# Kernel optimization log

Measured on AMD Instinct MI355X. Metric: run time of the kernel, lower is better.

Reference implementation:

```python
import jax, jax.numpy as jnp
import numpy as np

V, E, H = 50000, 256, 256   # vocab, emb_dim, hid_dim
R, S, W = 64, 32, 64        # reviews, sentences/review, words/sentence
UF = 20                     # user feature dim


def _bigru_last(x, wih, whh, bih, bhh):
    """Bidirectional GRU over x [B,T,D]; returns sum of final hidden states of
    the two directions, shape [B,H]. Params stacked over direction axis 0."""
    Hh = whh.shape[-1]

    def onedir(xd, wi, wh, bi, bh):
        gx = jnp.einsum('btd,gd->btg', xd, wi) + bi  # [B,T,3H] input gates precomputed

        def step(h, gxt):
            gh = h @ wh.T + bh
            r = jax.nn.sigmoid(gxt[:, :Hh] + gh[:, :Hh])
            z = jax.nn.sigmoid(gxt[:, Hh:2 * Hh] + gh[:, Hh:2 * Hh])
            n = jnp.tanh(gxt[:, 2 * Hh:] + r * gh[:, 2 * Hh:])
            return (1.0 - z) * n + z * h, None

        h0 = jnp.zeros((xd.shape[0], Hh), xd.dtype)
        hT, _ = jax.lax.scan(step, h0, jnp.swapaxes(gx, 0, 1))
        return hT

    return (onedir(x, wih[0], whh[0], bih[0], bhh[0])
            + onedir(x[:, ::-1], wih[1], whh[1], bih[1], bhh[1]))


def setup_inputs() -> dict:
    key = jax.random.key(0)
    ks = iter(jax.random.split(key, 40))

    def wmat(shape, scale=0.05):
        return jax.random.normal(next(ks), shape, jnp.float32) * scale

    inp = {}
    inp['inputs'] = jax.random.randint(next(ks), (R, S, W), 0, V)
    inp['sent_lengths'] = jax.random.randint(next(ks), (R, S), 1, W)
    inp['sent_counts'] = jax.random.randint(next(ks), (R,), 1, S)
    inp['user_feats'] = jax.random.normal(next(ks), (R, UF), jnp.float32)
    inp['embed'] = wmat((V, E))
    for name, din in (('wg', E), ('sg', H), ('rg', H + UF)):
        inp[name + '_wih'] = wmat((2, 3 * H, din))
        inp[name + '_whh'] = wmat((2, 3 * H, H))
        inp[name + '_bih'] = jnp.zeros((2, 3 * H), jnp.float32)
        inp[name + '_bhh'] = jnp.zeros((2, 3 * H), jnp.float32)
    inp['rfc_w1'] = wmat((H // 2, H + UF)); inp['rfc_b1'] = jnp.zeros((H // 2,), jnp.float32)
    inp['rfc_w2'] = wmat((1, H // 2));      inp['rfc_b2'] = jnp.zeros((1,), jnp.float32)
    inp['pfc_w1'] = wmat((H // 2, H));      inp['pfc_b1'] = jnp.zeros((H // 2,), jnp.float32)
    inp['pfc_w2'] = wmat((9, H // 2));      inp['pfc_b2'] = jnp.zeros((9,), jnp.float32)
    inp['uf_w'] = jnp.ones((UF,), jnp.float32)  # user_feats_weights
    return inp


def reference(inputs, sent_lengths, sent_counts, user_feats, embed,
              wg_wih, wg_whh, wg_bih, wg_bhh,
              sg_wih, sg_whh, sg_bih, sg_bhh,
              rg_wih, rg_whh, rg_bih, rg_bhh,
              rfc_w1, rfc_b1, rfc_w2, rfc_b2,
              pfc_w1, pfc_b1, pfc_w2, pfc_b2, uf_w):
    Rr, Sr, Wr = inputs.shape
    emb = embed[inputs]  # [R,S,W,E]  (dropout = identity in eval mode)
    # word-level bi-GRU, all R*S sentences batched together
    sent = _bigru_last(emb.reshape(Rr * Sr, Wr, emb.shape[-1]),
                       wg_wih, wg_whh, wg_bih, wg_bhh).reshape(Rr, Sr, -1)
    # sentence-level bi-GRU, batch over reviews
    rev = _bigru_last(sent, sg_wih, sg_whh, sg_bih, sg_bhh)  # [R,H]
    # F.normalize(user_feats) * user_feats_weights
    nrm = jnp.maximum(jnp.linalg.norm(user_feats, axis=-1, keepdims=True), 1e-12)
    p_batch = jnp.concatenate([rev, (user_feats / nrm) * uf_w], axis=-1)  # [R,H+20]
    r_stars = (jax.nn.selu(p_batch @ rfc_w1.T + rfc_b1) @ rfc_w2.T + rfc_b2)[:, 0]  # [R]
    # review-level bi-GRU over the sequence of reviews (batch 1)
    doc = _bigru_last(p_batch[None], rg_wih, rg_whh, rg_bih, rg_bhh)[0]  # [H]
    p_stars = jax.nn.selu(doc @ pfc_w1.T + pfc_b1) @ pfc_w2.T + pfc_b2  # [9]
    return p_stars, r_stars
```

## Files before the change

kernel.cpp:

```cpp
#include <hip/hip_runtime.h>
#include <math.h>

#define R_ 64
#define S_ 32
#define W_ 64
#define H_ 256
#define UF_ 20
#define TC 4

typedef short bf16x8 __attribute__((ext_vector_type(8)));
typedef float f32x4  __attribute__((ext_vector_type(4)));

#define MFMA(a,b,c) __builtin_amdgcn_mfma_f32_16x16x32_bf16((a),(b),(c),0,0,0)

#define BFRAG(ff) ((ff) < 40 ? Breg[(ff) < 40 ? (ff) : 0] \
                 : *(const bf16x8*)&Bl[w][(ff) >= 40 ? (ff)-40 : 0][l*8])

__device__ __forceinline__ float sigf(float x){ return 1.0f/(1.0f+__expf(-x)); }
__device__ __forceinline__ float tanhf_(float x){ float e=__expf(2.0f*x); return 1.0f-2.0f/(e+1.0f); }
__device__ __forceinline__ float seluf_(float x){
  const float sc=1.0507009873554805f, al=1.6732632423543772f;
  return x>0.0f ? sc*x : sc*al*(expf(x)-1.0f);
}
__device__ __forceinline__ short tobf(float f){
  unsigned u=__float_as_uint(f); u += 0x7fffu + ((u>>16)&1u); return (short)(u>>16);
}
__device__ __forceinline__ float bf2f(short s){
  return __uint_as_float(((unsigned)(unsigned short)s) << 16);
}
__device__ __forceinline__ unsigned pk2(float a, float b){
  return (unsigned)(unsigned short)tobf(a) | ((unsigned)(unsigned short)tobf(b) << 16);
}

__global__ void prep_word_w(const float* __restrict__ wih, const float* __restrict__ whh,
                            short* __restrict__ Bw)
{
  int idx = blockIdx.x*256 + threadIdx.x;
  int lane = idx & 63;
  int rest = idx >> 6;
  int f  = rest % 6;  rest /= 6;
  int kt = rest % 16; rest /= 16;
  int w  = rest % 8;
  int d  = rest / 8;
  int gate = f >> 1;
  int j = 32*w + (f&1)*16 + (lane&15);
  int row = gate*256 + j;
  const float* W = (kt < 8 ? wih : whh) + (size_t)d*768*256;
  int k = (kt&7)*32 + (lane>>4)*8;
  short* dst = Bw + ((((size_t)(d*8 + w)*16 + kt)*6 + f)*64 + lane)*8;
#pragma unroll
  for (int jj=0;jj<8;jj++) dst[jj] = tobf(W[(size_t)row*256 + k + jj]);
}

__global__ void prep_rnn_w(const float* __restrict__ whh, short* __restrict__ Bs)
{
  int idx = blockIdx.x*256 + threadIdx.x;
  int lane = idx & 63;
  int rest = idx >> 6;
  int f  = rest % 6; rest /= 6;
  int kt = rest % 8; rest /= 8;
  int w  = rest % 8;
  int d  = rest / 8;
  int j = 32*w + (f&1)*16 + (lane&15);
  int row = (f>>1)*256 + j;
  const float* W = whh + (size_t)d*768*256;
  int k = kt*32 + (lane>>4)*8;
  short* dst = Bs + ((((size_t)(d*8 + w)*8 + kt)*6 + f)*64 + lane)*8;
#pragma unroll
  for (int jj=0;jj<8;jj++) dst[jj] = tobf(W[(size_t)row*256 + k + jj]);
}

__global__ void prep_gemm_w(const float* __restrict__ Wsrc, short* __restrict__ Bg)
{
  int idx = blockIdx.x*256 + threadIdx.x;
  int lane = idx & 63;
  int rest = idx >> 6;
  int kt = rest % 8;
  int nt = rest / 8;
  int n = nt*16 + (lane&15);
  int k = kt*32 + (lane>>4)*8;
  short* dst = Bg + (((size_t)nt*8 + kt)*64 + lane)*8;
#pragma unroll
  for (int jj=0;jj<8;jj++) dst[jj] = tobf(Wsrc[(size_t)n*256 + k + jj]);
}

__global__ __launch_bounds__(256) void gemm_gxu(
    const short* __restrict__ Ab, const float* __restrict__ Af,
    const int* __restrict__ toks, const short* __restrict__ Bg,
    const float* __restrict__ bih, const float* __restrict__ bhh,
    short* __restrict__ C, long Czoff,
    int mode, int t0, int Mclamp, int Cstride)
{
  const int z  = blockIdx.z;
  const int m0 = blockIdx.x * 64;
  const int yt = blockIdx.y * 8;
  const int ntb = (mode == 2 ? z*48 : 0) + yt;
  const int tid = threadIdx.x;
  const int w = tid >> 6, l = tid & 63;
  const int c = l & 15, q = l >> 4;
  __shared__ short As[64][264];
  {
    const int row = tid >> 2, c0 = (tid & 3) * 64;
    if (mode == 0) {
      const uint4* s = (const uint4*)(Ab + (size_t)(m0+row)*256 + c0);
#pragma unroll
      for (int i = 0; i < 8; i++) *(uint4*)&As[row][c0 + i*8] = s[i];
    } else {
      int r;
      if (mode == 1) {
        r = m0 + row; if (r >= Mclamp) r = Mclamp - 1;
      } else {
        const int rr = m0 + row;
        const int s_ = rr / TC, i_ = rr % TC;
        const int wd = z ? (63 - (t0 + i_)) : (t0 + i_);
        r = toks[s_*64 + wd];
      }
      const float* s = Af + (size_t)r*256 + c0;
#pragma unroll
      for (int i = 0; i < 8; i++) {
        float4 v0 = *(const float4*)(s + i*8);
        float4 v1 = *(const float4*)(s + i*8 + 4);
        uint4 u;
        u.x = pk2(v0.x, v0.y); u.y = pk2(v0.z, v0.w);
        u.z = pk2(v1.x, v1.y); u.w = pk2(v1.z, v1.w);
        *(uint4*)&As[row][c0 + i*8] = u;
      }
    }
  }
  float bias[2];
#pragma unroll
  for (int nt = 0; nt < 2; nt++) {
    const int coln = (yt + 2*w + nt)*16 + c;
    const int bidx = (mode == 2 ? z*768 : 0) + coln;
    bias[nt] = bih[bidx] + ((bidx % 768) < 512 ? bhh[bidx] : 0.0f);
  }
  __syncthreads();
  f32x4 acc[4][2];
#pragma unroll
  for (int a = 0; a < 4; a++) { acc[a][0] = (f32x4)0.f; acc[a][1] = (f32x4)0.f; }
#pragma unroll
  for (int kt = 0; kt < 8; kt++) {
    const int ko = kt*32 + q*8;
    bf16x8 a0 = *(const bf16x8*)&As[ 0+c][ko];
    bf16x8 a1 = *(const bf16x8*)&As[16+c][ko];
    bf16x8 a2 = *(const bf16x8*)&As[32+c][ko];
    bf16x8 a3 = *(const bf16x8*)&As[48+c][ko];
    bf16x8 b0 = *(const bf16x8*)&Bg[(((size_t)(ntb + 2*w    )*8 + kt)*64 + l)*8];
    bf16x8 b1 = *(const bf16x8*)&Bg[(((size_t)(ntb + 2*w + 1)*8 + kt)*64 + l)*8];
    acc[0][0]=MFMA(a0,b0,acc[0][0]); acc[1][0]=MFMA(a1,b0,acc[1][0]);
    acc[2][0]=MFMA(a2,b0,acc[2][0]); acc[3][0]=MFMA(a3,b0,acc[3][0]);
    acc[0][1]=MFMA(a0,b1,acc[0][1]); acc[1][1]=MFMA(a1,b1,acc[1][1]);
    acc[2][1]=MFMA(a2,b1,acc[2][1]); acc[3][1]=MFMA(a3,b1,acc[3][1]);
  }
  short* Cz = C + (size_t)z * Czoff;
#pragma unroll
  for (int mt = 0; mt < 4; mt++)
#pragma unroll
  for (int nt = 0; nt < 2; nt++)
#pragma unroll
  for (int rg = 0; rg < 4; rg++)
    Cz[(size_t)(m0 + mt*16 + q*4 + rg)*Cstride + (yt + 2*w + nt)*16 + c] =
        tobf(acc[mt][nt][rg] + bias[nt]);
}

__global__ __launch_bounds__(512, 2) void gru_rec(
    const int* __restrict__ toks,
    const short* __restrict__ gxF, const short* __restrict__ gxB,
    const short* __restrict__ Bh, int wstride, int koff,
    const float* __restrict__ bhh,
    float* __restrict__ hstate, int NS,
    int t0, int nsteps, int mode, int nwords)
{
  const int d = blockIdx.x & 1;
  const int g = blockIdx.x >> 1;
  const int tid = threadIdx.x;
  const int w = tid >> 6, l = tid & 63;
  const int c = l & 15, q = l >> 4;
  const int j0 = 32*w + c;

  __shared__ short hbf[2][16][256];
  __shared__ short Bl[8][8][512];
  __shared__ int   tokL[1024];

  if (mode == 0)
    for (int i = tid; i < 1024; i += 512) tokL[i] = toks[(size_t)g*1024 + i];

  bf16x8 Breg[40];
  {
    const short* Bb = Bh + (size_t)(d*8 + w)*wstride + (size_t)koff*3072 + l*8;
#pragma unroll
    for (int ff = 0; ff < 48; ff++) {
      bf16x8 v = *(const bf16x8*)(Bb + ff*512);
      if (ff < 40) Breg[ff] = v;
      else *(bf16x8*)&Bl[w][ff-40][l*8] = v;
    }
  }

  float bNH[2];
#pragma unroll
  for (int jt = 0; jt < 2; jt++)
    bNH[jt] = bhh[d*768 + 512 + j0 + jt*16];

  float hst[2][4];
  const int cur0 = t0 & 1;
  if (t0 == 0) {
#pragma unroll
    for (int a = 0; a < 2; a++)
#pragma unroll
    for (int r = 0; r < 4; r++) hst[a][r] = 0.0f;
  } else {
#pragma unroll
    for (int jt = 0; jt < 2; jt++)
#pragma unroll
    for (int rg = 0; rg < 4; rg++)
      hst[jt][rg] = hstate[((size_t)d*NS + g*16 + q*4 + rg)*256 + j0 + jt*16];
  }
#pragma unroll
  for (int jt = 0; jt < 2; jt++)
#pragma unroll
  for (int rg = 0; rg < 4; rg++) {
    const int m = q*4 + rg;
    hbf[cur0][m][(j0 + jt*16) ^ ((m&7)<<3)] = tobf(hst[jt][rg]);
  }

  __syncthreads();

  const int tend = t0 + nsteps;
  for (int t = t0; t < tend; t++) {
    const int cur = t & 1, nxt = 1 - cur;

    const short* rb[4];
#pragma unroll
    for (int rg = 0; rg < 4; rg++) {
      const int m = q*4 + rg;
      if (mode == 0) {
        const int tx = d ? (nwords - 1 - t) : t;
        rb[rg] = gxF + (size_t)tokL[m*64 + tx]*1536 + d*768 + j0;
      } else if (mode == 1) {
        const int ri = (g*16 + m)*TC + (t - t0);
        rb[rg] = (d ? gxB : gxF) + (size_t)ri*768 + j0;
      } else {
        const int se = d ? (nwords - 1 - t) : t;
        rb[rg] = gxF + ((size_t)(g*16 + m)*nwords + se)*1536 + d*768 + j0;
      }
    }
    short Gv[4][2][3];
#pragma unroll
    for (int rg = 0; rg < 4; rg++)
#pragma unroll
    for (int jt = 0; jt < 2; jt++)
#pragma unroll
    for (int ga = 0; ga < 3; ga++)
      Gv[rg][jt][ga] = rb[rg][ga*256 + jt*16];

    f32x4 accR[2], accZ[2], accNH[2];
#pragma unroll
    for (int a = 0; a < 2; a++) { accR[a]=(f32x4)0.f; accZ[a]=(f32x4)0.f; accNH[a]=(f32x4)0.f; }
#pragma unroll
    for (int kt = 0; kt < 8; kt++) {
      bf16x8 a0 = *(const bf16x8*)&hbf[cur][c][(kt*32 + q*8) ^ ((c&7)<<3)];
      bf16x8 b0 = BFRAG(kt*6+0), b1 = BFRAG(kt*6+1), b2 = BFRAG(kt*6+2),
             b3 = BFRAG(kt*6+3), b4 = BFRAG(kt*6+4), b5 = BFRAG(kt*6+5);
      accR[0]=MFMA(a0,b0,accR[0]);  accR[1]=MFMA(a0,b1,accR[1]);
      accZ[0]=MFMA(a0,b2,accZ[0]);  accZ[1]=MFMA(a0,b3,accZ[1]);
      accNH[0]=MFMA(a0,b4,accNH[0]); accNH[1]=MFMA(a0,b5,accNH[1]);
    }

#pragma unroll
    for (int jt = 0; jt < 2; jt++)
#pragma unroll
    for (int rg = 0; rg < 4; rg++) {
      const int m = q*4 + rg;
      const float r = sigf(bf2f(Gv[rg][jt][0]) + accR[jt][rg]);
      const float z = sigf(bf2f(Gv[rg][jt][1]) + accZ[jt][rg]);
      const float n = tanhf_(bf2f(Gv[rg][jt][2]) + r*(accNH[jt][rg] + bNH[jt]));
      const float h = n + z*(hst[jt][rg] - n);
      hst[jt][rg] = h;
      hbf[nxt][m][(j0 + jt*16) ^ ((m&7)<<3)] = tobf(h);
    }
    __syncthreads();
  }

#pragma unroll
  for (int jt = 0; jt < 2; jt++)
#pragma unroll
  for (int rg = 0; rg < 4; rg++)
    hstate[((size_t)d*NS + g*16 + q*4 + rg)*256 + j0 + jt*16] = hst[jt][rg];
}

__global__ void add2bf(const float* __restrict__ a, const float* __restrict__ b,
                       short* __restrict__ o)
{
  int i = (blockIdx.x*256 + threadIdx.x)*4;
  float4 x = *(const float4*)&a[i];
  float4 y = *(const float4*)&b[i];
  *(uint2*)&o[i] = make_uint2(pk2(x.x+y.x, x.y+y.y), pk2(x.z+y.z, x.w+y.w));
}

__global__ __launch_bounds__(512, 2) void rev_gru(
    const float* __restrict__ gx, const short* __restrict__ Br,
    const float* __restrict__ bhh,
    float* __restrict__ doc)
{
  const int d = blockIdx.x;
  const int tid = threadIdx.x;
  const int w = tid >> 6, l = tid & 63;
  const int c = l & 15, q = l >> 4;
  const int j0 = 32*w + c;

  __shared__ short hbf[2][16][256];
  __shared__ short Bl[8][8][512];
  for (int i = tid; i < 2*16*256; i += 512) ((short*)hbf)[i] = 0;

  bf16x8 Breg[40];
  {
    const short* Bbase = Br + (size_t)(d*8 + w)*8*6*512 + l*8;
#pragma unroll
    for (int ff = 0; ff < 48; ff++) {
      bf16x8 v = *(const bf16x8*)(Bbase + ff*512);
      if (ff < 40) Breg[ff] = v;
      else *(bf16x8*)&Bl[w][ff-40][l*8] = v;
    }
  }

  float bNH[2];
#pragma unroll
  for (int jt = 0; jt < 2; jt++)
    bNH[jt] = bhh[d*768 + 512 + j0 + jt*16];

  float hst[2];
  hst[0] = 0.0f; hst[1] = 0.0f;
  __syncthreads();

  for (int t = 0; t < 64; t++) {
    const int cur = t & 1, nxt = 1 - cur;
    const int teff = (d == 0) ? t : (63 - t);

    float G[2][3];
    if (q == 0) {
#pragma unroll
      for (int jt = 0; jt < 2; jt++) {
        const size_t row = (size_t)teff*1536 + d*768;
        const int j = j0 + jt*16;
        G[jt][0] = gx[row + j]; G[jt][1] = gx[row + 256 + j]; G[jt][2] = gx[row + 512 + j];
      }
    }

    f32x4 accR[2], accZ[2], accNH[2];
#pragma unroll
    for (int a=0;a<2;a++) { accR[a]=(f32x4)0.f; accZ[a]=(f32x4)0.f; accNH[a]=(f32x4)0.f; }
#pragma unroll
    for (int kt = 0; kt < 8; kt++) {
      bf16x8 a0 = *(const bf16x8*)&hbf[cur][c][(kt*32 + q*8) ^ ((c&7)<<3)];
      bf16x8 b0 = BFRAG(kt*6+0), b1 = BFRAG(kt*6+1), b2 = BFRAG(kt*6+2),
             b3 = BFRAG(kt*6+3), b4 = BFRAG(kt*6+4), b5 = BFRAG(kt*6+5);
      accR[0]=MFMA(a0,b0,accR[0]);  accR[1]=MFMA(a0,b1,accR[1]);
      accZ[0]=MFMA(a0,b2,accZ[0]);  accZ[1]=MFMA(a0,b3,accZ[1]);
      accNH[0]=MFMA(a0,b4,accNH[0]); accNH[1]=MFMA(a0,b5,accNH[1]);
    }

    if (q == 0) {
#pragma unroll
      for (int jt = 0; jt < 2; jt++) {
        const float r = sigf(G[jt][0] + accR[jt][0]);
        const float z = sigf(G[jt][1] + accZ[jt][0]);
        const float n = tanhf_(G[jt][2] + r*(accNH[jt][0] + bNH[jt]));
        const float h = n + z*(hst[jt] - n);
        hst[jt] = h;
        hbf[nxt][0][j0 + jt*16] = tobf(h);
      }
    }
    __syncthreads();
  }
  if (q == 0) {
#pragma unroll
    for (int jt = 0; jt < 2; jt++)
      doc[d*256 + j0 + jt*16] = hst[jt];
  }
}

__global__ __launch_bounds__(256) void gemm_nt16(
    const float* __restrict__ A, const float* __restrict__ B,
    const float* __restrict__ bih, const float* __restrict__ bhh,
    float* __restrict__ C, int M, int N, int K)
{
  const int m0 = blockIdx.x * 16;
  const int n0 = blockIdx.y * 64;
  const int tid = threadIdx.x;
  __shared__ float As[16][17];
  __shared__ float Bs[16][68];
  float acc[4] = {0,0,0,0};
  const int m  = tid >> 4, n4 = (tid & 15) * 4;
  const int bn = tid >> 2, bk = (tid & 3) * 4;
  for (int k0 = 0; k0 < K; k0 += 16) {
    const int ak = tid & 15;
    float av = (k0 + ak < K) ? A[(size_t)(m0+m)*K + k0 + ak] : 0.0f;
    float4 b4 = make_float4(0,0,0,0);
    if (k0 + bk < K) b4 = *(const float4*)&B[(size_t)(n0+bn)*K + k0 + bk];
    __syncthreads();
    As[ak][m] = av;
    Bs[bk+0][bn]=b4.x; Bs[bk+1][bn]=b4.y; Bs[bk+2][bn]=b4.z; Bs[bk+3][bn]=b4.w;
    __syncthreads();
#pragma unroll
    for (int k = 0; k < 16; k++) {
      const float a = As[k][m];
      const float4 bb = *(const float4*)&Bs[k][n4];
      acc[0]+=a*bb.x; acc[1]+=a*bb.y; acc[2]+=a*bb.z; acc[3]+=a*bb.w;
    }
  }
#pragma unroll
  for (int i = 0; i < 4; i++) {
    const int n = n0 + n4 + i;
    acc[i] += bih[n] + ((n % 768) < 512 ? bhh[n] : 0.0f);
  }
  *(float4*)&C[(size_t)(m0+m)*N + n0+n4] = make_float4(acc[0],acc[1],acc[2],acc[3]);
}

__global__ void pbatch_k(const float* __restrict__ hs, const float* __restrict__ uf,
                         const float* __restrict__ ufw, float* __restrict__ pb)
{
  const int r = blockIdx.x, tid = threadIdx.x;
  __shared__ float nrm;
  if (tid == 0) {
    float s = 0.f;
    for (int i = 0; i < UF_; i++) { const float v = uf[r*UF_ + i]; s += v*v; }
    nrm = fmaxf(sqrtf(s), 1e-12f);
  }
  __syncthreads();
  if (tid < H_)  pb[r*276 + tid] = hs[r*H_ + tid] + hs[(size_t)R_*H_ + r*H_ + tid];
  if (tid < UF_) pb[r*276 + H_ + tid] = uf[r*UF_ + tid] / nrm * ufw[tid];
}

__global__ void rstars_k(const float* __restrict__ pb,
                         const float* __restrict__ w1, const float* __restrict__ b1,
                         const float* __restrict__ w2, const float* __restrict__ b2,
                         float* __restrict__ out)
{
  const int r = blockIdx.x, tid = threadIdx.x;
  __shared__ float ps[276];
  __shared__ float s1[128];
  for (int i = tid; i < 276; i += 128) ps[i] = pb[r*276 + i];
  __syncthreads();
  float a = b1[tid];
  for (int k = 0; k < 276; k++) a += ps[k] * w1[tid*276 + k];
  s1[tid] = seluf_(a);
  __syncthreads();
  if (tid == 0) {
    float s = b2[0];
    for (int k = 0; k < 128; k++) s += s1[k] * w2[k];
    out[9 + r] = s;
  }
}

__global__ void pstars_k(const float* __restrict__ doc2,
                         const float* __restrict__ w1, const float* __restrict__ b1,
                         const float* __restrict__ w2, const float* __restrict__ b2,
                         float* __restrict__ out)
{
  const int tid = threadIdx.x;
  __shared__ float dc[256];
  __shared__ float s1[128];
  dc[tid]       = doc2[tid];
  dc[128 + tid] = doc2[128 + tid];
  __syncthreads();
  float a = b1[tid];
  for (int k = 0; k < 256; k++) a += dc[k] * w1[tid*256 + k];
  s1[tid] = seluf_(a);
  __syncthreads();
  if (tid < 9) {
    float s = b2[tid];
    for (int k = 0; k < 128; k++) s += s1[k] * w2[tid*128 + k];
    out[tid] = s;
  }
}

__global__ void docsum_k(float* __restrict__ doc)
{
  const int tid = threadIdx.x;
  doc[tid] = doc[tid] + doc[256 + tid];
}

extern "C" void kernel_launch(void* const* d_in, const int* in_sizes, int n_in,
                              void* d_out, int out_size, void* d_ws, size_t ws_size,
                              hipStream_t stream)
{
  const int*   toks   = (const int*)  d_in[0];
  const float* uf     = (const float*)d_in[3];
  const float* embed  = (const float*)d_in[4];
  const float* wg_wih = (const float*)d_in[5];
  const float* wg_whh = (const float*)d_in[6];
  const float* wg_bih = (const float*)d_in[7];
  const float* wg_bhh = (const float*)d_in[8];
  const float* sg_wih = (const float*)d_in[9];
  const float* sg_whh = (const float*)d_in[10];
  const float* sg_bih = (const float*)d_in[11];
  const float* sg_bhh = (const float*)d_in[12];
  const float* rg_wih = (const float*)d_in[13];
  const float* rg_whh = (const float*)d_in[14];
  const float* rg_bih = (const float*)d_in[15];
  const float* rg_bhh = (const float*)d_in[16];
  const float* rfc_w1 = (const float*)d_in[17];
  const float* rfc_b1 = (const float*)d_in[18];
  const float* rfc_w2 = (const float*)d_in[19];
  const float* rfc_b2 = (const float*)d_in[20];
  const float* pfc_w1 = (const float*)d_in[21];
  const float* pfc_b1 = (const float*)d_in[22];
  const float* pfc_w2 = (const float*)d_in[23];
  const float* pfc_b2 = (const float*)d_in[24];
  const float* uf_w   = (const float*)d_in[25];
  float* out = (float*)d_out;
  float* ws  = (float*)d_ws;
  (void)in_sizes; (void)n_in; (void)out_size;

  const size_t OFF_BW   = 0;
  const size_t OFF_BS   = OFF_BW  + 393216;
  const size_t OFF_BR   = OFF_BS  + 196608;
  const size_t OFF_BG   = OFF_BR  + 196608;
  const size_t OFF_BGW  = OFF_BG  + 196608;
  const size_t OFF_HF   = OFF_BGW + 196608;
  const size_t OFF_SB   = OFF_HF  + 1048576;
  const size_t OFF_GXS  = OFF_SB  + 262144;
  const size_t OFF_HS   = OFF_GXS + 1572864;
  const size_t OFF_PB   = OFF_HS  + 32768;
  const size_t OFF_GXR  = OFF_PB  + 17664;
  const size_t OFF_DOC  = OFF_GXR + 98304;
  const size_t OFF_GXT  = OFF_DOC + 512;
  const size_t TOT_A    = OFF_GXT + (size_t)50048*1536/2;

  short* Bw   = (short*)(ws + OFF_BW);
  short* Bs   = (short*)(ws + OFF_BS);
  short* Br   = (short*)(ws + OFF_BR);
  short* Bg   = (short*)(ws + OFF_BG);
  short* Bgw  = (short*)(ws + OFF_BGW);
  float* hfin = ws + OFF_HF;
  short* sentb= (short*)(ws + OFF_SB);
  short* gxs  = (short*)(ws + OFF_GXS);
  float* hs   = ws + OFF_HS;
  float* pb   = ws + OFF_PB;
  float* gxr  = ws + OFF_GXR;
  float* doc  = ws + OFF_DOC;
  short* gxf  = (short*)(ws + OFF_GXT);
  short* gxb  = gxf + (size_t)8192*768;
  short* gxv  = (short*)(ws + OFF_GXT);

  const bool big = ws_size >= TOT_A * sizeof(float);

  prep_word_w<<<384, 256, 0, stream>>>(wg_wih, wg_whh, Bw);
  prep_rnn_w<<<192, 256, 0, stream>>>(sg_whh, Bs);
  prep_rnn_w<<<192, 256, 0, stream>>>(rg_whh, Br);
  prep_gemm_w<<<192, 256, 0, stream>>>(sg_wih, Bg);
  prep_gemm_w<<<192, 256, 0, stream>>>(wg_wih, Bgw);

  if (big) {
    gemm_gxu<<<dim3(782, 12, 1), 256, 0, stream>>>(
        nullptr, embed, nullptr, Bgw, wg_bih, wg_bhh, gxv, 0, 1, 0, 50000, 1536);
    gru_rec<<<256, 512, 0, stream>>>(toks, gxv, nullptr, Bw, 49152, 8,
        wg_bhh, hfin, 2048, 0, 64, 0, 64);
  } else {
    for (int tc = 0; tc < 64/TC; tc++) {
      gemm_gxu<<<dim3(128, 6, 2), 256, 0, stream>>>(
          nullptr, embed, toks, Bgw, wg_bih, wg_bhh, gxf, (long)8192*768, 2, tc*TC, 0, 768);
      gru_rec<<<256, 512, 0, stream>>>(toks, gxf, gxb, Bw, 49152, 8,
          wg_bhh, hfin, 2048, tc*TC, TC, 1, 64);
    }
  }
  add2bf<<<512, 256, 0, stream>>>(hfin, hfin + (size_t)2048*256, sentb);

  gemm_gxu<<<dim3(32, 12, 1), 256, 0, stream>>>(
      sentb, nullptr, nullptr, Bg, sg_bih, sg_bhh, gxs, 0, 0, 0, 2048, 1536);
  gru_rec<<<8, 512, 0, stream>>>(nullptr, gxs, nullptr, Bs, 24576, 0,
      sg_bhh, hs, 64, 0, 32, 2, 32);

  pbatch_k<<<R_, 256, 0, stream>>>(hs, uf, uf_w, pb);
  rstars_k<<<R_, 128, 0, stream>>>(pb, rfc_w1, rfc_b1, rfc_w2, rfc_b2, out);

  gemm_nt16<<<dim3(4, 24), 256, 0, stream>>>(pb, rg_wih, rg_bih, rg_bhh, gxr, 64, 1536, 276);
  rev_gru<<<2, 512, 0, stream>>>(gxr, Br, rg_bhh, doc);
  docsum_k<<<1, 256, 0, stream>>>(doc);
  pstars_k<<<1, 128, 0, stream>>>(doc, pfc_w1, pfc_b1, pfc_w2, pfc_b2, out);
}
```

Baseline: 805.1 us.

## Prefetch next-step gate inputs into LDS asynchronously in the GRU recurrence

```diff
diff --git a/kernel.cpp b/kernel.cpp
--- a/kernel.cpp
+++ b/kernel.cpp
@@ -12,6 +12,13 @@
 typedef float f32x4  __attribute__((ext_vector_type(4)));
 
 #define MFMA(a,b,c) __builtin_amdgcn_mfma_f32_16x16x32_bf16((a),(b),(c),0,0,0)
+
+typedef const unsigned int __attribute__((address_space(1)))* gp_t;
+typedef unsigned int __attribute__((address_space(3)))* lp_t;
+#define GLOAD16(SRC, DST) \
+  __builtin_amdgcn_global_load_lds((gp_t)(const void*)(SRC), (lp_t)(void*)(DST), 16, 0, 0)
+
+#define SW(r) ((((r)>>1)&7)<<3)
 
 #define BFRAG(ff) ((ff) < 40 ? Breg[(ff) < 40 ? (ff) : 0] \
                  : *(const bf16x8*)&Bl[w][(ff) >= 40 ? (ff)-40 : 0][l*8])
@@ -163,6 +170,36 @@
         tobf(acc[mt][nt][rg] + bias[nt]);
 }
 
+__device__ __forceinline__ void stage_issue(
+    short* dstbase,
+    int mode, int d, int g, int w, int l,
+    int nwords, int t0, int tt,
+    const int* tokp, const short* gxF, const short* gxB)
+{
+  const char* bF = (const char*)gxF;
+  const char* bB = (const char*)gxB;
+#pragma unroll
+  for (int i = 0; i < 3; i++) {
+    const int off = i*1024 + l*16;
+    const int rl  = (off >= 1536) ? 1 : 0;
+    const int col = off - rl*1536;
+    const char* src;
+    if (mode == 0) {
+      const int tx  = d ? (nwords - 1 - tt) : tt;
+      const int tok = tokp[(2*w + rl)*64 + tx];
+      src = bF + (size_t)tok*3072 + d*1536 + col;
+    } else if (mode == 1) {
+      const int ri = (g*16 + 2*w + rl)*TC + (tt - t0);
+      src = (d ? bB : bF) + (size_t)ri*1536 + col;
+    } else {
+      const int se  = d ? (nwords - 1 - tt) : tt;
+      const int row = g*16 + 2*w + rl;
+      src = bF + ((size_t)row*nwords + se)*3072 + (size_t)d*1536 + col;
+    }
+    GLOAD16(src, dstbase + (size_t)w*1544 + i*512);
+  }
+}
+
 __global__ __launch_bounds__(512, 2) void gru_rec(
     const int* __restrict__ toks,
     const short* __restrict__ gxF, const short* __restrict__ gxB,
@@ -178,6 +215,7 @@
   const int c = l & 15, q = l >> 4;
   const int j0 = 32*w + c;
 
+  __shared__ short gbuf[2][8][1544];
   __shared__ short hbf[2][16][256];
   __shared__ short Bl[8][8][512];
   __shared__ int   tokL[1024];
@@ -220,8 +258,11 @@
 #pragma unroll
   for (int rg = 0; rg < 4; rg++) {
     const int m = q*4 + rg;
-    hbf[cur0][m][(j0 + jt*16) ^ ((m&7)<<3)] = tobf(hst[jt][rg]);
-  }
+    hbf[cur0][m][(j0 + jt*16) ^ SW(m)] = tobf(hst[jt][rg]);
+  }
+
+  stage_issue(&gbuf[cur0][0][0], mode, d, g, w, l, nwords, t0, t0,
+              (mode == 0) ? toks + (size_t)g*1024 : (const int*)nullptr, gxF, gxB);
 
   __syncthreads();
 
@@ -229,54 +270,60 @@
   for (int t = t0; t < tend; t++) {
     const int cur = t & 1, nxt = 1 - cur;
 
-    const short* rb[4];
+    if (t + 1 < tend)
+      stage_issue(&gbuf[nxt][0][0], mode, d, g, w, l, nwords, t0, t + 1,
+                  tokL, gxF, gxB);
+
+    bf16x8 areg[8];
+#pragma unroll
+    for (int kt = 0; kt < 8; kt++)
+      areg[kt] = *(const bf16x8*)&hbf[cur][c][(kt*32 + q*8) ^ SW(c)];
+
+    short Gv[4][2][3];
 #pragma unroll
     for (int rg = 0; rg < 4; rg++) {
       const int m = q*4 + rg;
-      if (mode == 0) {
-        const int tx = d ? (nwords - 1 - t) : t;
-        rb[rg] = gxF + (size_t)tokL[m*64 + tx]*1536 + d*768 + j0;
-      } else if (mode == 1) {
-        const int ri = (g*16 + m)*TC + (t - t0);
-        rb[rg] = (d ? gxB : gxF) + (size_t)ri*768 + j0;
-      } else {
-        const int se = d ? (nwords - 1 - t) : t;
-        rb[rg] = gxF + ((size_t)(g*16 + m)*nwords + se)*1536 + d*768 + j0;
-      }
-    }
-    short Gv[4][2][3];
-#pragma unroll
-    for (int rg = 0; rg < 4; rg++)
+      const short* gb = &gbuf[cur][0][0] + (m>>1)*1544 + (m&1)*768 + j0;
+#pragma unroll
+      for (int jt = 0; jt < 2; jt++)
+#pragma unroll
+      for (int ga = 0; ga < 3; ga++)
+        Gv[rg][jt][ga] = gb[ga*256 + jt*16];
+    }
+
+    f32x4 accR[2], accZ[2], accNH[2];
+#pragma unroll
+    for (int a = 0; a < 2; a++) { accR[a]=(f32x4)0.f; accZ[a]=(f32x4)0.f; accNH[a]=(f32x4)0.f; }
+#pragma unroll
+    for (int kt = 0; kt < 8; kt++) {
+      bf16x8 b0 = BFRAG(kt*6+0), b1 = BFRAG(kt*6+1),
+             b2 = BFRAG(kt*6+2), b3 = BFRAG(kt*6+3);
+      accR[0]=MFMA(areg[kt],b0,accR[0]);  accR[1]=MFMA(areg[kt],b1,accR[1]);
+      accZ[0]=MFMA(areg[kt],b2,accZ[0]);  accZ[1]=MFMA(areg[kt],b3,accZ[1]);
+    }
+#pragma unroll
+    for (int kt = 0; kt < 8; kt++) {
+      bf16x8 b4 = BFRAG(kt*6+4), b5 = BFRAG(kt*6+5);
+      accNH[0]=MFMA(areg[kt],b4,accNH[0]); accNH[1]=MFMA(areg[kt],b5,accNH[1]);
+    }
+
+    float rv[2][4], zv[2][4];
 #pragma unroll
     for (int jt = 0; jt < 2; jt++)
 #pragma unroll
-    for (int ga = 0; ga < 3; ga++)
-      Gv[rg][jt][ga] = rb[rg][ga*256 + jt*16];
-
-    f32x4 accR[2], accZ[2], accNH[2];
-#pragma unroll
-    for (int a = 0; a < 2; a++) { accR[a]=(f32x4)0.f; accZ[a]=(f32x4)0.f; accNH[a]=(f32x4)0.f; }
-#pragma unroll
-    for (int kt = 0; kt < 8; kt++) {
-      bf16x8 a0 = *(const bf16x8*)&hbf[cur][c][(kt*32 + q*8) ^ ((c&7)<<3)];
-      bf16x8 b0 = BFRAG(kt*6+0), b1 = BFRAG(kt*6+1), b2 = BFRAG(kt*6+2),
-             b3 = BFRAG(kt*6+3), b4 = BFRAG(kt*6+4), b5 = BFRAG(kt*6+5);
-      accR[0]=MFMA(a0,b0,accR[0]);  accR[1]=MFMA(a0,b1,accR[1]);
-      accZ[0]=MFMA(a0,b2,accZ[0]);  accZ[1]=MFMA(a0,b3,accZ[1]);
-      accNH[0]=MFMA(a0,b4,accNH[0]); accNH[1]=MFMA(a0,b5,accNH[1]);
-    }
-
+    for (int rg = 0; rg < 4; rg++) {
+      rv[jt][rg] = sigf(bf2f(Gv[rg][jt][0]) + accR[jt][rg]);
+      zv[jt][rg] = sigf(bf2f(Gv[rg][jt][1]) + accZ[jt][rg]);
+    }
 #pragma unroll
     for (int jt = 0; jt < 2; jt++)
 #pragma unroll
     for (int rg = 0; rg < 4; rg++) {
       const int m = q*4 + rg;
-      const float r = sigf(bf2f(Gv[rg][jt][0]) + accR[jt][rg]);
-      const float z = sigf(bf2f(Gv[rg][jt][1]) + accZ[jt][rg]);
-      const float n = tanhf_(bf2f(Gv[rg][jt][2]) + r*(accNH[jt][rg] + bNH[jt]));
-      const float h = n + z*(hst[jt][rg] - n);
+      const float n = tanhf_(bf2f(Gv[rg][jt][2]) + rv[jt][rg]*(accNH[jt][rg] + bNH[jt]));
+      const float h = n + zv[jt][rg]*(hst[jt][rg] - n);
       hst[jt][rg] = h;
-      hbf[nxt][m][(j0 + jt*16) ^ ((m&7)<<3)] = tobf(h);
+      hbf[nxt][m][(j0 + jt*16) ^ SW(m)] = tobf(h);
     }
     __syncthreads();
   }
@@ -346,17 +393,25 @@
       }
     }
 
+    bf16x8 areg[8];
+#pragma unroll
+    for (int kt = 0; kt < 8; kt++)
+      areg[kt] = *(const bf16x8*)&hbf[cur][c][(kt*32 + q*8) ^ SW(c)];
+
     f32x4 accR[2], accZ[2], accNH[2];
 #pragma unroll
     for (int a=0;a<2;a++) { accR[a]=(f32x4)0.f; accZ[a]=(f32x4)0.f; accNH[a]=(f32x4)0.f; }
 #pragma unroll
     for (int kt = 0; kt < 8; kt++) {
-      bf16x8 a0 = *(const bf16x8*)&hbf[cur][c][(kt*32 + q*8) ^ ((c&7)<<3)];
-      bf16x8 b0 = BFRAG(kt*6+0), b1 = BFRAG(kt*6+1), b2 = BFRAG(kt*6+2),
-             b3 = BFRAG(kt*6+3), b4 = BFRAG(kt*6+4), b5 = BFRAG(kt*6+5);
-      accR[0]=MFMA(a0,b0,accR[0]);  accR[1]=MFMA(a0,b1,accR[1]);
-      accZ[0]=MFMA(a0,b2,accZ[0]);  accZ[1]=MFMA(a0,b3,accZ[1]);
-      accNH[0]=MFMA(a0,b4,accNH[0]); accNH[1]=MFMA(a0,b5,accNH[1]);
+      bf16x8 b0 = BFRAG(kt*6+0), b1 = BFRAG(kt*6+1),
+             b2 = BFRAG(kt*6+2), b3 = BFRAG(kt*6+3);
+      accR[0]=MFMA(areg[kt],b0,accR[0]);  accR[1]=MFMA(areg[kt],b1,accR[1]);
+      accZ[0]=MFMA(areg[kt],b2,accZ[0]);  accZ[1]=MFMA(areg[kt],b3,accZ[1]);
+    }
+#pragma unroll
+    for (int kt = 0; kt < 8; kt++) {
+      bf16x8 b4 = BFRAG(kt*6+4), b5 = BFRAG(kt*6+5);
+      accNH[0]=MFMA(areg[kt],b4,accNH[0]); accNH[1]=MFMA(areg[kt],b5,accNH[1]);
     }
 
     if (q == 0) {
```

Measured after the change: 753.9 us. 6.4% less time.

## Prefetch GRU input-gate rows into double-buffered LDS with async global_load_lds

Applied to the files above, without the earlier changes.

```diff
diff --git a/kernel.cpp b/kernel.cpp
--- a/kernel.cpp
+++ b/kernel.cpp
@@ -12,6 +12,13 @@
 typedef float f32x4  __attribute__((ext_vector_type(4)));
 
 #define MFMA(a,b,c) __builtin_amdgcn_mfma_f32_16x16x32_bf16((a),(b),(c),0,0,0)
+
+typedef const unsigned int __attribute__((address_space(1)))* gp_t;
+typedef unsigned int __attribute__((address_space(3)))* lp_t;
+#define GLOAD16(SRC, DST) \
+  __builtin_amdgcn_global_load_lds((gp_t)(const void*)(SRC), (lp_t)(void*)(DST), 16, 0, 0)
+
+#define SW(r) ((((r)>>1)&7)<<3)
 
 #define BFRAG(ff) ((ff) < 40 ? Breg[(ff) < 40 ? (ff) : 0] \
                  : *(const bf16x8*)&Bl[w][(ff) >= 40 ? (ff)-40 : 0][l*8])
@@ -163,6 +170,36 @@
         tobf(acc[mt][nt][rg] + bias[nt]);
 }
 
+__device__ __forceinline__ void stage_issue(
+    short* dstbase,
+    int mode, int d, int g, int w, int l,
+    int nwords, int t0, int tt,
+    const int* tokp, const short* gxF, const short* gxB)
+{
+  const char* bF = (const char*)gxF;
+  const char* bB = (const char*)gxB;
+#pragma unroll
+  for (int i = 0; i < 3; i++) {
+    const int off = i*1024 + l*16;
+    const int rl  = (off >= 1536) ? 1 : 0;
+    const int col = off - rl*1536;
+    const char* src;
+    if (mode == 0) {
+      const int tx  = d ? (nwords - 1 - tt) : tt;
+      const int tok = tokp[(2*w + rl)*64 + tx];
+      src = bF + (size_t)tok*3072 + d*1536 + col;
+    } else if (mode == 1) {
+      const int ri = (g*16 + 2*w + rl)*TC + (tt - t0);
+      src = (d ? bB : bF) + (size_t)ri*1536 + col;
+    } else {
+      const int se  = d ? (nwords - 1 - tt) : tt;
+      const int row = g*16 + 2*w + rl;
+      src = bF + ((size_t)row*nwords + se)*3072 + (size_t)d*1536 + col;
+    }
+    GLOAD16(src, dstbase + (size_t)w*1536 + i*512);
+  }
+}
+
 __global__ __launch_bounds__(512, 2) void gru_rec(
     const int* __restrict__ toks,
     const short* __restrict__ gxF, const short* __restrict__ gxB,
@@ -176,9 +213,9 @@
   const int tid = threadIdx.x;
   const int w = tid >> 6, l = tid & 63;
   const int c = l & 15, q = l >> 4;
-  const int j0 = 32*w + c;
-
-  __shared__ short hbf[2][16][256];
+
+  __shared__ short gbuf[2][16][768];
+  __shared__ short hbf[2][16][264];
   __shared__ short Bl[8][8][512];
   __shared__ int   tokL[1024];
 
@@ -199,7 +236,7 @@
   float bNH[2];
 #pragma unroll
   for (int jt = 0; jt < 2; jt++)
-    bNH[jt] = bhh[d*768 + 512 + j0 + jt*16];
+    bNH[jt] = bhh[d*768 + 512 + 32*w + jt*16 + c];
 
   float hst[2][4];
   const int cur0 = t0 & 1;
@@ -213,15 +250,16 @@
     for (int jt = 0; jt < 2; jt++)
 #pragma unroll
     for (int rg = 0; rg < 4; rg++)
-      hst[jt][rg] = hstate[((size_t)d*NS + g*16 + q*4 + rg)*256 + j0 + jt*16];
+      hst[jt][rg] = hstate[((size_t)d*NS + g*16 + q*4 + rg)*256 + 32*w + jt*16 + c];
   }
 #pragma unroll
   for (int jt = 0; jt < 2; jt++)
 #pragma unroll
-  for (int rg = 0; rg < 4; rg++) {
-    const int m = q*4 + rg;
-    hbf[cur0][m][(j0 + jt*16) ^ ((m&7)<<3)] = tobf(hst[jt][rg]);
-  }
+  for (int rg = 0; rg < 4; rg++)
+    hbf[cur0][q*4 + rg][32*w + jt*16 + c] = tobf(hst[jt][rg]);
+
+  stage_issue((short*)gbuf[cur0], mode, d, g, w, l, nwords, t0, t0,
+              (mode == 0) ? toks + (size_t)g*1024 : (const int*)nullptr, gxF, gxB);
 
   __syncthreads();
 
@@ -229,36 +267,16 @@
   for (int t = t0; t < tend; t++) {
     const int cur = t & 1, nxt = 1 - cur;
 
-    const short* rb[4];
-#pragma unroll
-    for (int rg = 0; rg < 4; rg++) {
-      const int m = q*4 + rg;
-      if (mode == 0) {
-        const int tx = d ? (nwords - 1 - t) : t;
-        rb[rg] = gxF + (size_t)tokL[m*64 + tx]*1536 + d*768 + j0;
-      } else if (mode == 1) {
-        const int ri = (g*16 + m)*TC + (t - t0);
-        rb[rg] = (d ? gxB : gxF) + (size_t)ri*768 + j0;
-      } else {
-        const int se = d ? (nwords - 1 - t) : t;
-        rb[rg] = gxF + ((size_t)(g*16 + m)*nwords + se)*1536 + d*768 + j0;
-      }
-    }
-    short Gv[4][2][3];
-#pragma unroll
-    for (int rg = 0; rg < 4; rg++)
-#pragma unroll
-    for (int jt = 0; jt < 2; jt++)
-#pragma unroll
-    for (int ga = 0; ga < 3; ga++)
-      Gv[rg][jt][ga] = rb[rg][ga*256 + jt*16];
+    if (t + 1 < tend)
+      stage_issue((short*)gbuf[nxt], mode, d, g, w, l, nwords, t0, t + 1,
+                  tokL, gxF, gxB);
 
     f32x4 accR[2], accZ[2], accNH[2];
 #pragma unroll
     for (int a = 0; a < 2; a++) { accR[a]=(f32x4)0.f; accZ[a]=(f32x4)0.f; accNH[a]=(f32x4)0.f; }
 #pragma unroll
     for (int kt = 0; kt < 8; kt++) {
-      bf16x8 a0 = *(const bf16x8*)&hbf[cur][c][(kt*32 + q*8) ^ ((c&7)<<3)];
+      bf16x8 a0 = *(const bf16x8*)&hbf[cur][c][kt*32 + q*8];
       bf16x8 b0 = BFRAG(kt*6+0), b1 = BFRAG(kt*6+1), b2 = BFRAG(kt*6+2),
              b3 = BFRAG(kt*6+3), b4 = BFRAG(kt*6+4), b5 = BFRAG(kt*6+5);
       accR[0]=MFMA(a0,b0,accR[0]);  accR[1]=MFMA(a0,b1,accR[1]);
@@ -271,12 +289,17 @@
 #pragma unroll
     for (int rg = 0; rg < 4; rg++) {
       const int m = q*4 + rg;
-      const float r = sigf(bf2f(Gv[rg][jt][0]) + accR[jt][rg]);
-      const float z = sigf(bf2f(Gv[rg][jt][1]) + accZ[jt][rg]);
-      const float n = tanhf_(bf2f(Gv[rg][jt][2]) + r*(accNH[jt][rg] + bNH[jt]));
-      const float h = n + z*(hst[jt][rg] - n);
+      const int j = 32*w + jt*16 + c;
+      const float gr = bf2f(gbuf[cur][m][j]);
+      const float gz = bf2f(gbuf[cur][m][256 + j]);
+      const float gn = bf2f(gbuf[cur][m][512 + j]);
+      const float r = sigf(gr + accR[jt][rg]);
+      const float z = sigf(gz + accZ[jt][rg]);
+      const float n = tanhf_(gn + r*(accNH[jt][rg] + bNH[jt]));
+      float h = hst[jt][rg];
+      h = (1.0f - z)*n + z*h;
       hst[jt][rg] = h;
-      hbf[nxt][m][(j0 + jt*16) ^ ((m&7)<<3)] = tobf(h);
+      hbf[nxt][m][j] = tobf(h);
     }
     __syncthreads();
   }
@@ -285,7 +308,7 @@
   for (int jt = 0; jt < 2; jt++)
 #pragma unroll
   for (int rg = 0; rg < 4; rg++)
-    hstate[((size_t)d*NS + g*16 + q*4 + rg)*256 + j0 + jt*16] = hst[jt][rg];
+    hstate[((size_t)d*NS + g*16 + q*4 + rg)*256 + 32*w + jt*16 + c] = hst[jt][rg];
 }
 
 __global__ void add2bf(const float* __restrict__ a, const float* __restrict__ b,
@@ -351,7 +374,7 @@
     for (int a=0;a<2;a++) { accR[a]=(f32x4)0.f; accZ[a]=(f32x4)0.f; accNH[a]=(f32x4)0.f; }
 #pragma unroll
     for (int kt = 0; kt < 8; kt++) {
-      bf16x8 a0 = *(const bf16x8*)&hbf[cur][c][(kt*32 + q*8) ^ ((c&7)<<3)];
+      bf16x8 a0 = *(const bf16x8*)&hbf[cur][c][(kt*32 + q*8) ^ SW(c)];
       bf16x8 b0 = BFRAG(kt*6+0), b1 = BFRAG(kt*6+1), b2 = BFRAG(kt*6+2),
              b3 = BFRAG(kt*6+3), b4 = BFRAG(kt*6+4), b5 = BFRAG(kt*6+5);
       accR[0]=MFMA(a0,b0,accR[0]);  accR[1]=MFMA(a0,b1,accR[1]);
```

After: 706.3 us. -12.3%, faster.
